# Performance work log

Hardware: AMD Instinct MI355X
Metric: run time of the kernel (lower is better)

Reference implementation:

```python
import jax, jax.numpy as jnp
import numpy as np

NUM_HEADS = 16

def setup_inputs() -> dict:
    key = jax.random.key(0)
    k1, k2, k3 = jax.random.split(key, 3)
    B, S, D = 2, 2048, 1024
    return {
        "hidden_states": jax.random.normal(k1, (B, S, D), dtype=jnp.float32),
        "W_attn": jax.random.normal(k2, (D, 3 * D), dtype=jnp.float32) * 0.02,
        "b_attn": jnp.zeros((3 * D,), dtype=jnp.float32),
        "W_proj": jax.random.normal(k3, (D, D), dtype=jnp.float32) * 0.02,
        "b_proj": jnp.zeros((D,), dtype=jnp.float32),
    }

def reference(hidden_states, W_attn, b_attn, W_proj, b_proj):
    B, S, D = hidden_states.shape
    H = NUM_HEADS
    hd = D // H
    # qkv projection (Conv1D == addmm): [B,S,3D]
    qkv = hidden_states @ W_attn + b_attn
    q, k, v = jnp.split(qkv, 3, axis=-1)
    # split heads -> [B,H,S,hd]
    def split_heads(t):
        return t.reshape(B, S, H, hd).transpose(0, 2, 1, 3)
    q, k, v = split_heads(q), split_heads(k), split_heads(v)
    # scaled QK^T: [B,H,S,S]
    scores = jnp.einsum('bhqd,bhkd->bhqk', q, k) / jnp.asarray(hd ** 0.5, dtype=q.dtype)
    causal = jnp.tril(jnp.ones((S, S), dtype=bool))
    mask_value = jnp.finfo(scores.dtype).min
    scores = jnp.where(causal, scores, mask_value)
    probs = jax.nn.softmax(scores, axis=-1)  # attn_pdrop=0 -> no dropout
    out = jnp.einsum('bhqk,bhkd->bhqd', probs, v)
    # merge heads -> [B,S,D]
    out = out.transpose(0, 2, 1, 3).reshape(B, S, D)
    out = out @ W_proj + b_proj  # resid_pdrop=0 -> no dropout
    return out
```

## Files before the change

kernel.cpp:

```cpp
#include <hip/hip_runtime.h>
#include <math.h>

typedef __attribute__((ext_vector_type(8))) short bf16x8;
typedef __attribute__((ext_vector_type(4))) short bf16x4;
typedef __attribute__((ext_vector_type(4))) float f32x4;
typedef __attribute__((ext_vector_type(16))) float f32x16;

#define MFMA16(a, b, c) __builtin_amdgcn_mfma_f32_16x16x32_bf16(a, b, c, 0, 0, 0)
#define MFMA32(a, b, c) __builtin_amdgcn_mfma_f32_32x32x16_bf16(a, b, c, 0, 0, 0)

#define GLOAD_LDS16(g, l)                                                        \
    __builtin_amdgcn_global_load_lds(                                            \
        (const __attribute__((address_space(1))) void*)(g),                      \
        (__attribute__((address_space(3))) void*)(l), 16, 0, 0)

__device__ __forceinline__ short f2bf(float f) {
    union { float f; unsigned u; } x; x.f = f;
    unsigned r = (x.u + 0x7fffu + ((x.u >> 16) & 1u)) >> 16;
    return (short)r;
}

__device__ __forceinline__ f32x16 zero16() {
    f32x16 z;
#pragma unroll
    for (int i = 0; i < 16; i++) z[i] = 0.f;
    return z;
}

__global__ __launch_bounds__(256) void convert_bf16_kernel(
    const float* __restrict__ in, short* __restrict__ out, int n4) {
    int i = blockIdx.x * 256 + threadIdx.x;
    if (i >= n4) return;
    float4 v = ((const float4*)in)[i];
    bf16x4 o;
    o[0] = f2bf(v.x); o[1] = f2bf(v.y); o[2] = f2bf(v.z); o[3] = f2bf(v.w);
    ((bf16x4*)out)[i] = o;
}

__global__ __launch_bounds__(256) void transpose_w2_kernel(
    const float* __restrict__ Wa, const float* __restrict__ Wp,
    short* __restrict__ WaT, short* __restrict__ WpT) {
    __shared__ float tile[32][33];
    const float* W; short* Wt; int N, xb;
    if (blockIdx.x < 96) { W = Wa; Wt = WaT; N = 3072; xb = blockIdx.x; }
    else                 { W = Wp; Wt = WpT; N = 1024; xb = blockIdx.x - 96; }
    const int K = 1024;
    int c = threadIdx.x & 31, r0 = threadIdx.x >> 5;
    int n0 = xb << 5, k0 = blockIdx.y << 5;
#pragma unroll
    for (int i = 0; i < 4; i++) {
        int r = r0 + i * 8;
        tile[r][c] = W[(long)(k0 + r) * N + n0 + c];
    }
    __syncthreads();
#pragma unroll
    for (int i = 0; i < 4; i++) {
        int r = r0 + i * 8;
        Wt[(long)(n0 + r) * K + k0 + c] = f2bf(tile[c][r]);
    }
}

template <int EPI>
__global__ __launch_bounds__(256) void gemm_bt_kernel(
    const short* __restrict__ A, const short* __restrict__ Bt,
    const float* __restrict__ bias, float* __restrict__ outF,
    short* __restrict__ qkv, short* __restrict__ VTb,
    int M, int N, int Kdim) {
    __shared__ __align__(16) short lsAll[17408];
    short* lsA = lsAll;
    short* lsB = lsAll + 8192;
    const int tid = threadIdx.x;
    const int lane = tid & 63, l15 = lane & 15, quad = lane >> 4;
    const int w = tid >> 6, wm = w >> 1, wn = w & 1;
    const int m0 = blockIdx.y * 128, n0 = blockIdx.x * 128;
    const int e = l15 & 7;
    const int lrow = lane >> 3;
    const int lgcol = ((lane & 7) ^ lrow) << 3;

    f32x4 acc[4][4];
#pragma unroll
    for (int i = 0; i < 4; i++)
#pragma unroll
        for (int j = 0; j < 4; j++) acc[i][j] = (f32x4){0.f, 0.f, 0.f, 0.f};

    for (int k0 = 0; k0 < Kdim; k0 += 64) {
#pragma unroll
        for (int ii = 0; ii < 4; ii++) {
            const int i = (w << 2) + ii;
            const int grow = (i << 3) + lrow;
            GLOAD_LDS16(&A[(size_t)(m0 + grow) * Kdim + k0 + lgcol], &lsA[i * 512]);
            GLOAD_LDS16(&Bt[(size_t)(n0 + grow) * Kdim + k0 + lgcol], &lsB[i * 512]);
        }
        __syncthreads();
#pragma unroll
        for (int kk = 0; kk < 64; kk += 32) {
            const int kb = kk >> 3;
            bf16x8 af[4], bfr[4];
#pragma unroll
            for (int t = 0; t < 4; t++) {
                const int sw = (((kb + quad) ^ e) << 3);
                af[t] = *(const bf16x8*)&lsA[(wm * 64 + t * 16 + l15) * 64 + sw];
                bfr[t] = *(const bf16x8*)&lsB[(wn * 64 + t * 16 + l15) * 64 + sw];
            }
#pragma unroll
            for (int mt = 0; mt < 4; mt++)
#pragma unroll
                for (int nt = 0; nt < 4; nt++)
                    acc[mt][nt] = MFMA16(af[mt], bfr[nt], acc[mt][nt]);
        }
        __syncthreads();
    }

    if (EPI == 0) {
#pragma unroll
        for (int nt = 0; nt < 4; nt++) {
            int nn = n0 + wn * 64 + nt * 16 + l15;
            float bv = bias[nn];
#pragma unroll
            for (int mt = 0; mt < 4; mt++)
#pragma unroll
                for (int r = 0; r < 4; r++) {
                    int mm = m0 + wm * 64 + mt * 16 + quad * 4 + r;
                    outF[(long)mm * N + nn] = acc[mt][nt][r] + bv;
                }
        }
    } else if (n0 < 2048) {
        const float scale = (n0 < 1024) ? 0.18033688011112042f : 1.0f;
#pragma unroll
        for (int nt = 0; nt < 4; nt++) {
            int nn = n0 + wn * 64 + nt * 16 + l15;
            float bv = bias[nn];
#pragma unroll
            for (int mt = 0; mt < 4; mt++)
#pragma unroll
                for (int r = 0; r < 4; r++) {
                    int mm = m0 + wm * 64 + mt * 16 + quad * 4 + r;
                    qkv[(long)mm * 3072 + nn] = f2bf((acc[mt][nt][r] + bv) * scale);
                }
        }
    } else {
        short* vt = &lsAll[w * (64 * 68)];
#pragma unroll
        for (int nt = 0; nt < 4; nt++) {
            int nn = n0 + wn * 64 + nt * 16 + l15;
            float bv = bias[nn];
#pragma unroll
            for (int mt = 0; mt < 4; mt++) {
                bf16x4 pk;
#pragma unroll
                for (int r = 0; r < 4; r++) pk[r] = f2bf(acc[mt][nt][r] + bv);
                *(bf16x4*)&vt[(nt * 16 + l15) * 68 + mt * 16 + quad * 4] = pk;
            }
        }
        const int hh = ((n0 - 2048) >> 6) + wn;
        const int bb = m0 >> 11;
        const int srow = (m0 & 2047) + wm * 64;
        const int sloc = (lane & 7) << 3;
#pragma unroll
        for (int i = 0; i < 8; i++) {
            const int d = i * 8 + (lane >> 3);
            bf16x8 vv = *(const bf16x8*)&vt[d * 68 + sloc];
            *(bf16x8*)&VTb[((size_t)(bb * 16 + hh) * 64 + d) * 2048 + srow + sloc] = vv;
        }
    }
}

__global__ __launch_bounds__(256, 3) void attn_kernel(
    const short* __restrict__ qkv, const short* __restrict__ VT,
    short* __restrict__ Ao) {
    __shared__ __align__(16) short Kt[2][64 * 64];
    __shared__ __align__(16) short Vt[2][64 * 64];
    __shared__ __align__(16) short Pt[4][32 * 64];
    const int tid = threadIdx.x;
    const int lane = tid & 63, col = lane & 31, hi = lane >> 5, w = tid >> 6;
    const int bx = blockIdx.x;
    const int qt = 15 - (bx >> 5);
    const int hb = bx & 31;
    const int b = hb >> 4, h = hb & 15;
    const size_t rowbase = (size_t)b * 2048 * 3072 + h * 64;
    const short* Qb = qkv + rowbase;
    const short* Kb = qkv + rowbase + 1024;
    const short* Vh = VT + (size_t)hb * 64 * 2048;
    short* Pw = &Pt[w][0];

    const int srow0 = tid >> 3, sc40 = (tid & 7) ^ (srow0 & 7);
    const int srow1 = srow0 + 32, sc41 = (tid & 7) ^ (srow1 & 7);
    const int sdst0 = srow0 * 64 + ((tid & 7) << 3);
    const int sdst1 = srow1 * 64 + ((tid & 7) << 3);

    const int qloc = w * 32 + col;
    const int qglob = qt * 128 + qloc;

    bf16x8 qf[4];
#pragma unroll
    for (int kc = 0; kc < 4; kc++)
        qf[kc] = *(const bf16x8*)&Qb[(long)qglob * 3072 + kc * 16 + hi * 8];

    float l = 0.f;
    f32x16 o[2];
    o[0] = zero16(); o[1] = zero16();

    const int nc = 2 * qt + 2;
    const int ca = 2 * qt + (w >> 1);

    *(bf16x8*)&Kt[0][sdst0] = *(const bf16x8*)&Kb[(size_t)srow0 * 3072 + sc40 * 8];
    *(bf16x8*)&Kt[0][sdst1] = *(const bf16x8*)&Kb[(size_t)srow1 * 3072 + sc41 * 8];
    *(bf16x8*)&Vt[0][sdst0] = *(const bf16x8*)&Vh[srow0 * 2048 + sc40 * 8];
    *(bf16x8*)&Vt[0][sdst1] = *(const bf16x8*)&Vh[srow1 * 2048 + sc41 * 8];
    __syncthreads();

    for (int c = 0; c < nc; c++) {
        const short* Kc = &Kt[c & 1][0];
        const short* Vc = &Vt[c & 1][0];
        const bool more = (c + 1 < nc);
        bf16x8 kr0, kr1, vr0, vr1;
        if (more) {
            const int k2 = (c + 1) * 64;
            kr0 = *(const bf16x8*)&Kb[(size_t)(k2 + srow0) * 3072 + sc40 * 8];
            kr1 = *(const bf16x8*)&Kb[(size_t)(k2 + srow1) * 3072 + sc41 * 8];
            vr0 = *(const bf16x8*)&Vh[srow0 * 2048 + k2 + sc40 * 8];
            vr1 = *(const bf16x8*)&Vh[srow1 * 2048 + k2 + sc41 * 8];
        }

        if (c <= ca) {
            f32x16 s[2];
#pragma unroll
            for (int t = 0; t < 2; t++) {
                f32x16 z = zero16();
#pragma unroll
                for (int kc = 0; kc < 4; kc++) {
                    const int row = t * 32 + col;
                    bf16x8 kf = *(const bf16x8*)&Kc[row * 64 + (((kc * 2 + hi) ^ (row & 7)) << 3)];
                    z = MFMA32(kf, qf[kc], z);
                }
                s[t] = z;
            }

            if (c == ca) {
#pragma unroll
                for (int t = 0; t < 2; t++) {
                    const int thresh = qloc + qt * 128 - c * 64 - t * 32;
#pragma unroll
                    for (int g = 0; g < 4; g++)
#pragma unroll
                        for (int r2 = 0; r2 < 4; r2++) {
                            const int row = r2 + 8 * g + 4 * hi;
                            if (row > thresh) s[t][g * 4 + r2] = -INFINITY;
                        }
                }
            }

#pragma unroll
            for (int t = 0; t < 2; t++) {
#pragma unroll
                for (int g = 0; g < 4; g++) {
                    bf16x4 pw;
#pragma unroll
                    for (int r2 = 0; r2 < 4; r2++) {
                        float pv = __builtin_amdgcn_exp2f(s[t][g * 4 + r2]);
                        l += pv;
                        pw[r2] = f2bf(pv);
                    }
                    *(bf16x4*)&Pw[col * 64 + (((t * 4 + g) ^ (col & 7)) << 3) + hi * 4] = pw;
                }
            }

            bf16x8 pf[4];
#pragma unroll
            for (int kc2 = 0; kc2 < 4; kc2++)
                pf[kc2] = *(const bf16x8*)&Pw[col * 64 + (((kc2 * 2 + hi) ^ (col & 7)) << 3)];

#pragma unroll
            for (int dt = 0; dt < 2; dt++) {
                const int vrow = dt * 32 + col;
#pragma unroll
                for (int kc2 = 0; kc2 < 4; kc2++) {
                    bf16x8 vf = *(const bf16x8*)&Vc[vrow * 64 + (((kc2 * 2 + hi) ^ (vrow & 7)) << 3)];
                    o[dt] = MFMA32(vf, pf[kc2], o[dt]);
                }
            }
        }

        if (more) {
            short* Kn = &Kt[(c + 1) & 1][0];
            short* Vn = &Vt[(c + 1) & 1][0];
            *(bf16x8*)&Kn[sdst0] = kr0;
            *(bf16x8*)&Kn[sdst1] = kr1;
            *(bf16x8*)&Vn[sdst0] = vr0;
            *(bf16x8*)&Vn[sdst1] = vr1;
        }
        __syncthreads();
    }

    l += __shfl_xor(l, 32);
    const float rl = 1.f / l;

    const long base = ((long)(b * 2048 + qglob)) * 1024 + h * 64;
#pragma unroll
    for (int dt = 0; dt < 2; dt++) {
#pragma unroll
        for (int g = 0; g < 4; g++) {
            bf16x4 wv;
#pragma unroll
            for (int r2 = 0; r2 < 4; r2++) wv[r2] = f2bf(o[dt][g * 4 + r2] * rl);
            *(bf16x4*)&Ao[base + dt * 32 + g * 8 + hi * 4] = wv;
        }
    }
}

extern "C" void kernel_launch(void* const* d_in, const int* in_sizes, int n_in,
                              void* d_out, int out_size, void* d_ws, size_t ws_size,
                              hipStream_t stream) {
    const float* hs = (const float*)d_in[0];
    const float* W_attn = (const float*)d_in[1];
    const float* b_attn = (const float*)d_in[2];
    const float* W_proj = (const float*)d_in[3];
    const float* b_proj = (const float*)d_in[4];
    float* out = (float*)d_out;

    char* ws = (char*)d_ws;
    short* hs_bf = (short*)ws;
    short* attn_o = hs_bf;
    short* WaT = (short*)(ws + 8u * 1024 * 1024);
    short* WpT = (short*)(ws + 14u * 1024 * 1024);
    short* qkv = (short*)(ws + 16u * 1024 * 1024);
    short* VTb = (short*)(ws + 40u * 1024 * 1024);

    convert_bf16_kernel<<<4096, 256, 0, stream>>>(hs, hs_bf, 1048576);
    transpose_w2_kernel<<<dim3(128, 32), 256, 0, stream>>>(W_attn, W_proj, WaT, WpT);
    gemm_bt_kernel<1><<<dim3(24, 32), 256, 0, stream>>>(
        hs_bf, WaT, b_attn, nullptr, qkv, VTb, 4096, 3072, 1024);
    attn_kernel<<<512, 256, 0, stream>>>(qkv, VTb, attn_o);
    gemm_bt_kernel<0><<<dim3(8, 32), 256, 0, stream>>>(
        attn_o, WpT, b_proj, out, nullptr, nullptr, 4096, 1024, 1024);
}
```

Baseline: 195.4 us.

## Split causal attention along KV into chunks with atomic accumulation and combine pass

Causal attention work is split across the key dimension: long query tiles are divided into up to four KV segments of eight chunks each, which raises the grid from 512 to 1280 blocks and balances the triangular workload. Partial O and l are atomically added into zeroed fp32 buffers, and a new combine kernel normalises them and writes bf16. This relies on the fixed max-free exp2 softmax. The QKV buffer is compacted to a QK layout with stride 2048, and the output projection gets its own 128x64-tile kernel so it launches more blocks. The cost is the memset, fp32 atomics, an extra launch and extra traffic.

```diff
diff --git a/kernel.cpp b/kernel.cpp
--- a/kernel.cpp
+++ b/kernel.cpp
@@ -60,12 +60,10 @@
     }
 }
 
-template <int EPI>
-__global__ __launch_bounds__(256) void gemm_bt_kernel(
+__global__ __launch_bounds__(256) void gemm_qkv_kernel(
     const short* __restrict__ A, const short* __restrict__ Bt,
-    const float* __restrict__ bias, float* __restrict__ outF,
-    short* __restrict__ qkv, short* __restrict__ VTb,
-    int M, int N, int Kdim) {
+    const float* __restrict__ bias,
+    short* __restrict__ QK, short* __restrict__ VTb, int Kdim) {
     __shared__ __align__(16) short lsAll[17408];
     short* lsA = lsAll;
     short* lsB = lsAll + 8192;
@@ -111,7 +109,8 @@
         __syncthreads();
     }
 
-    if (EPI == 0) {
+    if (n0 < 2048) {
+        const float scale = (n0 < 1024) ? 0.18033688011112042f : 1.0f;
 #pragma unroll
         for (int nt = 0; nt < 4; nt++) {
             int nn = n0 + wn * 64 + nt * 16 + l15;
@@ -121,21 +120,7 @@
 #pragma unroll
                 for (int r = 0; r < 4; r++) {
                     int mm = m0 + wm * 64 + mt * 16 + quad * 4 + r;
-                    outF[(long)mm * N + nn] = acc[mt][nt][r] + bv;
-                }
-        }
-    } else if (n0 < 2048) {
-        const float scale = (n0 < 1024) ? 0.18033688011112042f : 1.0f;
-#pragma unroll
-        for (int nt = 0; nt < 4; nt++) {
-            int nn = n0 + wn * 64 + nt * 16 + l15;
-            float bv = bias[nn];
-#pragma unroll
-            for (int mt = 0; mt < 4; mt++)
-#pragma unroll
-                for (int r = 0; r < 4; r++) {
-                    int mm = m0 + wm * 64 + mt * 16 + quad * 4 + r;
-                    qkv[(long)mm * 3072 + nn] = f2bf((acc[mt][nt][r] + bv) * scale);
+                    QK[(long)mm * 2048 + nn] = f2bf((acc[mt][nt][r] + bv) * scale);
                 }
         }
     } else {
@@ -165,21 +150,97 @@
     }
 }
 
+__global__ __launch_bounds__(256) void gemm_proj_kernel(
+    const short* __restrict__ A, const short* __restrict__ Bt,
+    const float* __restrict__ bias, float* __restrict__ outF) {
+    __shared__ __align__(16) short lsA[128 * 64];
+    __shared__ __align__(16) short lsB[64 * 64];
+    const int tid = threadIdx.x;
+    const int lane = tid & 63, l15 = lane & 15, quad = lane >> 4, w = tid >> 6;
+    const int m0 = blockIdx.y * 128, n0 = blockIdx.x * 64;
+    const int e = l15 & 7;
+    const int lrow = lane >> 3;
+    const int lgcol = ((lane & 7) ^ lrow) << 3;
+
+    f32x4 acc[2][4];
+#pragma unroll
+    for (int i = 0; i < 2; i++)
+#pragma unroll
+        for (int j = 0; j < 4; j++) acc[i][j] = (f32x4){0.f, 0.f, 0.f, 0.f};
+
+    for (int k0 = 0; k0 < 1024; k0 += 64) {
+#pragma unroll
+        for (int ii = 0; ii < 4; ii++) {
+            const int i = (w << 2) + ii;
+            const int grow = (i << 3) + lrow;
+            GLOAD_LDS16(&A[(size_t)(m0 + grow) * 1024 + k0 + lgcol], &lsA[i * 512]);
+        }
+#pragma unroll
+        for (int ii = 0; ii < 2; ii++) {
+            const int i = (w << 1) + ii;
+            const int grow = (i << 3) + lrow;
+            GLOAD_LDS16(&Bt[(size_t)(n0 + grow) * 1024 + k0 + lgcol], &lsB[i * 512]);
+        }
+        __syncthreads();
+#pragma unroll
+        for (int kk = 0; kk < 64; kk += 32) {
+            const int kb = kk >> 3;
+            const int sw = (((kb + quad) ^ e) << 3);
+            bf16x8 af[2], bfr[4];
+#pragma unroll
+            for (int mt = 0; mt < 2; mt++)
+                af[mt] = *(const bf16x8*)&lsA[(w * 32 + mt * 16 + l15) * 64 + sw];
+#pragma unroll
+            for (int nt = 0; nt < 4; nt++)
+                bfr[nt] = *(const bf16x8*)&lsB[(nt * 16 + l15) * 64 + sw];
+#pragma unroll
+            for (int mt = 0; mt < 2; mt++)
+#pragma unroll
+                for (int nt = 0; nt < 4; nt++)
+                    acc[mt][nt] = MFMA16(af[mt], bfr[nt], acc[mt][nt]);
+        }
+        __syncthreads();
+    }
+
+#pragma unroll
+    for (int nt = 0; nt < 4; nt++) {
+        int nn = n0 + nt * 16 + l15;
+        float bv = bias[nn];
+#pragma unroll
+        for (int mt = 0; mt < 2; mt++)
+#pragma unroll
+            for (int r = 0; r < 4; r++) {
+                int mm = m0 + w * 32 + mt * 16 + quad * 4 + r;
+                outF[(long)mm * 1024 + nn] = acc[mt][nt][r] + bv;
+            }
+    }
+}
+
 __global__ __launch_bounds__(256, 3) void attn_kernel(
-    const short* __restrict__ qkv, const short* __restrict__ VT,
-    short* __restrict__ Ao) {
+    const short* __restrict__ QK, const short* __restrict__ VT,
+    short* __restrict__ Ao, float* __restrict__ O_acc, float* __restrict__ l_acc) {
     __shared__ __align__(16) short Kt[2][64 * 64];
     __shared__ __align__(16) short Vt[2][64 * 64];
     __shared__ __align__(16) short Pt[4][32 * 64];
     const int tid = threadIdx.x;
     const int lane = tid & 63, col = lane & 31, hi = lane >> 5, w = tid >> 6;
     const int bx = blockIdx.x;
-    const int qt = 15 - (bx >> 5);
     const int hb = bx & 31;
+    const int sid = 39 - (bx >> 5);
+    int qt, s;
+    if (sid < 4)       { qt = sid;                 s = 0; }
+    else if (sid < 12) { qt = 4 + ((sid - 4) >> 1);  s = (sid - 4) & 1; }
+    else if (sid < 24) { qt = 8 + (sid - 12) / 3;    s = (sid - 12) % 3; }
+    else               { qt = 12 + ((sid - 24) >> 2); s = (sid - 24) & 3; }
+    const int nct = 2 * qt + 2;
+    const int c0 = s * 8;
+    const int c1 = (c0 + 8 < nct) ? c0 + 8 : nct;
+    const bool single = (qt < 4);
+
     const int b = hb >> 4, h = hb & 15;
-    const size_t rowbase = (size_t)b * 2048 * 3072 + h * 64;
-    const short* Qb = qkv + rowbase;
-    const short* Kb = qkv + rowbase + 1024;
+    const size_t rowbase = (size_t)b * 2048 * 2048 + h * 64;
+    const short* Qb = QK + rowbase;
+    const short* Kb = QK + rowbase + 1024;
     const short* Vh = VT + (size_t)hb * 64 * 2048;
     short* Pw = &Pt[w][0];
 
@@ -194,36 +255,38 @@
     bf16x8 qf[4];
 #pragma unroll
     for (int kc = 0; kc < 4; kc++)
-        qf[kc] = *(const bf16x8*)&Qb[(long)qglob * 3072 + kc * 16 + hi * 8];
+        qf[kc] = *(const bf16x8*)&Qb[(long)qglob * 2048 + kc * 16 + hi * 8];
 
     float l = 0.f;
     f32x16 o[2];
     o[0] = zero16(); o[1] = zero16();
 
-    const int nc = 2 * qt + 2;
     const int ca = 2 * qt + (w >> 1);
 
-    *(bf16x8*)&Kt[0][sdst0] = *(const bf16x8*)&Kb[(size_t)srow0 * 3072 + sc40 * 8];
-    *(bf16x8*)&Kt[0][sdst1] = *(const bf16x8*)&Kb[(size_t)srow1 * 3072 + sc41 * 8];
-    *(bf16x8*)&Vt[0][sdst0] = *(const bf16x8*)&Vh[srow0 * 2048 + sc40 * 8];
-    *(bf16x8*)&Vt[0][sdst1] = *(const bf16x8*)&Vh[srow1 * 2048 + sc41 * 8];
+    {
+        const int kk0 = c0 * 64;
+        *(bf16x8*)&Kt[0][sdst0] = *(const bf16x8*)&Kb[(size_t)(kk0 + srow0) * 2048 + sc40 * 8];
+        *(bf16x8*)&Kt[0][sdst1] = *(const bf16x8*)&Kb[(size_t)(kk0 + srow1) * 2048 + sc41 * 8];
+        *(bf16x8*)&Vt[0][sdst0] = *(const bf16x8*)&Vh[srow0 * 2048 + kk0 + sc40 * 8];
+        *(bf16x8*)&Vt[0][sdst1] = *(const bf16x8*)&Vh[srow1 * 2048 + kk0 + sc41 * 8];
+    }
     __syncthreads();
 
-    for (int c = 0; c < nc; c++) {
+    for (int c = c0; c < c1; c++) {
         const short* Kc = &Kt[c & 1][0];
         const short* Vc = &Vt[c & 1][0];
-        const bool more = (c + 1 < nc);
+        const bool more = (c + 1 < c1);
         bf16x8 kr0, kr1, vr0, vr1;
         if (more) {
             const int k2 = (c + 1) * 64;
-            kr0 = *(const bf16x8*)&Kb[(size_t)(k2 + srow0) * 3072 + sc40 * 8];
-            kr1 = *(const bf16x8*)&Kb[(size_t)(k2 + srow1) * 3072 + sc41 * 8];
+            kr0 = *(const bf16x8*)&Kb[(size_t)(k2 + srow0) * 2048 + sc40 * 8];
+            kr1 = *(const bf16x8*)&Kb[(size_t)(k2 + srow1) * 2048 + sc41 * 8];
             vr0 = *(const bf16x8*)&Vh[srow0 * 2048 + k2 + sc40 * 8];
             vr1 = *(const bf16x8*)&Vh[srow1 * 2048 + k2 + sc41 * 8];
         }
 
         if (c <= ca) {
-            f32x16 s[2];
+            f32x16 sx[2];
 #pragma unroll
             for (int t = 0; t < 2; t++) {
                 f32x16 z = zero16();
@@ -233,7 +296,7 @@
                     bf16x8 kf = *(const bf16x8*)&Kc[row * 64 + (((kc * 2 + hi) ^ (row & 7)) << 3)];
                     z = MFMA32(kf, qf[kc], z);
                 }
-                s[t] = z;
+                sx[t] = z;
             }
 
             if (c == ca) {
@@ -245,7 +308,7 @@
 #pragma unroll
                         for (int r2 = 0; r2 < 4; r2++) {
                             const int row = r2 + 8 * g + 4 * hi;
-                            if (row > thresh) s[t][g * 4 + r2] = -INFINITY;
+                            if (row > thresh) sx[t][g * 4 + r2] = -INFINITY;
                         }
                 }
             }
@@ -257,7 +320,7 @@
                     bf16x4 pw;
 #pragma unroll
                     for (int r2 = 0; r2 < 4; r2++) {
-                        float pv = __builtin_amdgcn_exp2f(s[t][g * 4 + r2]);
+                        float pv = __builtin_amdgcn_exp2f(sx[t][g * 4 + r2]);
                         l += pv;
                         pw[r2] = f2bf(pv);
                     }
@@ -292,20 +355,54 @@
         __syncthreads();
     }
 
-    l += __shfl_xor(l, 32);
-    const float rl = 1.f / l;
-
-    const long base = ((long)(b * 2048 + qglob)) * 1024 + h * 64;
-#pragma unroll
-    for (int dt = 0; dt < 2; dt++) {
-#pragma unroll
-        for (int g = 0; g < 4; g++) {
-            bf16x4 wv;
-#pragma unroll
-            for (int r2 = 0; r2 < 4; r2++) wv[r2] = f2bf(o[dt][g * 4 + r2] * rl);
-            *(bf16x4*)&Ao[base + dt * 32 + g * 8 + hi * 4] = wv;
-        }
-    }
+    if (single) {
+        l += __shfl_xor(l, 32);
+        const float rl = 1.f / l;
+        const long base = ((long)(b * 2048 + qglob)) * 1024 + h * 64;
+#pragma unroll
+        for (int dt = 0; dt < 2; dt++) {
+#pragma unroll
+            for (int g = 0; g < 4; g++) {
+                bf16x4 wv;
+#pragma unroll
+                for (int r2 = 0; r2 < 4; r2++) wv[r2] = f2bf(o[dt][g * 4 + r2] * rl);
+                *(bf16x4*)&Ao[base + dt * 32 + g * 8 + hi * 4] = wv;
+            }
+        }
+    } else {
+        l += __shfl_xor(l, 32);
+        const size_t obase = ((size_t)hb * 1536 + (qglob - 512)) * 64;
+#pragma unroll
+        for (int dt = 0; dt < 2; dt++)
+#pragma unroll
+            for (int g = 0; g < 4; g++)
+#pragma unroll
+                for (int r2 = 0; r2 < 4; r2++) {
+                    const int d = dt * 32 + g * 8 + hi * 4 + r2;
+                    unsafeAtomicAdd(&O_acc[obase + d], o[dt][g * 4 + r2]);
+                }
+        if (hi == 0) unsafeAtomicAdd(&l_acc[hb * 1536 + (qglob - 512)], l);
+    }
+}
+
+__global__ __launch_bounds__(256) void attn_combine_kernel(
+    const float* __restrict__ O_acc, const float* __restrict__ l_acc,
+    short* __restrict__ Ao) {
+    const int g = blockIdx.x * 256 + threadIdx.x;
+    const int row = g >> 2;
+    const int ds = (g & 3) << 4;
+    const int hb = row / 1536, qm = row - hb * 1536;
+    const int b = hb >> 4, h = hb & 15;
+    const float rl = 1.f / l_acc[row];
+    const float* src = &O_acc[(size_t)row * 64 + ds];
+    bf16x8 w0, w1;
+#pragma unroll
+    for (int i = 0; i < 8; i++) w0[i] = f2bf(src[i] * rl);
+#pragma unroll
+    for (int i = 0; i < 8; i++) w1[i] = f2bf(src[8 + i] * rl);
+    const long dst = ((long)(b * 2048 + qm + 512)) * 1024 + h * 64 + ds;
+    *(bf16x8*)&Ao[dst] = w0;
+    *(bf16x8*)&Ao[dst + 8] = w1;
 }
 
 extern "C" void kernel_launch(void* const* d_in, const int* in_sizes, int n_in,
@@ -318,19 +415,22 @@
     const float* b_proj = (const float*)d_in[4];
     float* out = (float*)d_out;
 
+    const size_t MB = 1024 * 1024;
     char* ws = (char*)d_ws;
     short* hs_bf = (short*)ws;
     short* attn_o = hs_bf;
-    short* WaT = (short*)(ws + 8u * 1024 * 1024);
-    short* WpT = (short*)(ws + 14u * 1024 * 1024);
-    short* qkv = (short*)(ws + 16u * 1024 * 1024);
-    short* VTb = (short*)(ws + 40u * 1024 * 1024);
+    float* O_acc = (float*)(ws + 8 * MB);
+    short* WaT = (short*)(ws + 8 * MB);
+    float* l_acc = (float*)(ws + 20 * MB);
+    short* WpT = (short*)(ws + 20 * MB + 256 * 1024);
+    short* QK = (short*)(ws + 22 * MB + 256 * 1024);
+    short* VTb = (short*)(ws + 38 * MB + 256 * 1024);
 
     convert_bf16_kernel<<<4096, 256, 0, stream>>>(hs, hs_bf, 1048576);
     transpose_w2_kernel<<<dim3(128, 32), 256, 0, stream>>>(W_attn, W_proj, WaT, WpT);
-    gemm_bt_kernel<1><<<dim3(24, 32), 256, 0, stream>>>(
-        hs_bf, WaT, b_attn, nullptr, qkv, VTb, 4096, 3072, 1024);
-    attn_kernel<<<512, 256, 0, stream>>>(qkv, VTb, attn_o);
-    gemm_bt_kernel<0><<<dim3(8, 32), 256, 0, stream>>>(
-        attn_o, WpT, b_proj, out, nullptr, nullptr, 4096, 1024, 1024);
-}
+    gemm_qkv_kernel<<<dim3(24, 32), 256, 0, stream>>>(hs_bf, WaT, b_attn, QK, VTb, 1024);
+    hipMemsetAsync(ws + 8 * MB, 0, 12 * MB + 192 * 1024, stream);
+    attn_kernel<<<1280, 256, 0, stream>>>(QK, VTb, attn_o, O_acc, l_acc);
+    attn_combine_kernel<<<768, 256, 0, stream>>>(O_acc, l_acc, attn_o);
+    gemm_proj_kernel<<<dim3(16, 32), 256, 0, stream>>>(attn_o, WpT, b_proj, out);
+}
```

Measured after the change: 400.4 us. 2.05x slower.
